# Performance work log

Measured on AMD Instinct MI355X. Metric: run time of the kernel, lower is better.

The kernel has to match this reference:

```python
import jax, jax.numpy as jnp
import numpy as np
from jax import lax


def setup_inputs() -> dict:
    key = jax.random.key(0)
    ks = jax.random.split(key, 16)
    def rn(k, shape, s=0.05):
        return (jax.random.normal(k, shape) * s).astype(jnp.float32)
    B, N, F = 16, 1024, 200
    return dict(
        x=jax.random.normal(ks[0], (B, 1, N, F), dtype=jnp.float32),
        gat_W=rn(ks[1], (F, F)), att_src=rn(ks[2], (F,)), att_dst=rn(ks[3], (F,)), gat_b=rn(ks[4], (F,)),
        conv1_w=rn(ks[5], (40, 1, 1, 26)), conv1_b=rn(ks[6], (40,)),
        bn1_g=jnp.ones((40,), jnp.float32), bn1_b=jnp.zeros((40,), jnp.float32),
        bn1_m=jnp.zeros((40,), jnp.float32), bn1_v=jnp.ones((40,), jnp.float32),
        conv2_w=rn(ks[7], (40, 40, N), 0.01), conv2_b=rn(ks[8], (40,)),
        bn2_g=jnp.ones((40,), jnp.float32), bn2_b=jnp.zeros((40,), jnp.float32),
        bn2_m=jnp.zeros((40,), jnp.float32), bn2_v=jnp.ones((40,), jnp.float32),
        projc_w=rn(ks[9], (40, 40)), projc_b=rn(ks[10], (40,)),
        W1=rn(ks[11], (1400, 1024)), b1=rn(ks[12], (1024,)),
        W2=rn(ks[13], (1024, 1024)), b2=rn(ks[14], (1024,)),
        ln_g=jnp.ones((1024,), jnp.float32), ln_b=jnp.zeros((1024,), jnp.float32),
    )


def _bn(y, g, b, m, v, eps=1e-5):
    # eval-mode BatchNorm over channel axis 1
    shp = (1, -1) + (1,) * (y.ndim - 2)
    return (y - m.reshape(shp)) * (g.reshape(shp) / jnp.sqrt(v.reshape(shp) + eps)) + b.reshape(shp)


def reference(x, gat_W, att_src, att_dst, gat_b, conv1_w, conv1_b,
              bn1_g, bn1_b, bn1_m, bn1_v, conv2_w, conv2_b,
              bn2_g, bn2_b, bn2_m, bn2_v, projc_w, projc_b,
              W1, b1, W2, b2, ln_g, ln_b):
    B, _, N, F = x.shape  # (16,1,1024,200)
    # --- EEG_GAT (PyG GATConv, heads=1). edge_index only covers nodes 0..N-1;
    # add_self_loops applies to all B*N nodes -> first graph is dense attention
    # (complete graph incl. self), remaining nodes see only their self-loop.
    h = x.reshape(B * N, F) @ gat_W               # (B*N, 200)
    a_s = h[:N] @ att_src                          # source scores, first graph
    a_d = h[:N] @ att_dst                          # target scores
    logits = jax.nn.leaky_relu(a_s[None, :] + a_d[:, None], 0.2)  # [target i, source j]
    out0 = jax.nn.softmax(logits, axis=1) @ h[:N]  # (N, 200)
    gat = (jnp.concatenate([out0, h[N:]], axis=0) + gat_b).reshape(B, 1, N, F)
    x = x + gat  # ResidualAdd (dropout in eval = identity)
    # --- PatchEmbedding shallownet
    y = lax.conv_general_dilated(x, conv1_w, (1, 1), 'VALID',
                                 dimension_numbers=('NCHW', 'OIHW', 'NCHW'))
    y = y + conv1_b[None, :, None, None]           # (B,40,1024,175)
    y = y.reshape(B, 40, N, 35, 5).mean(-1)        # AvgPool2d (1,5) stride (1,5)
    y = jax.nn.elu(_bn(y, bn1_g, bn1_b, bn1_m, bn1_v))
    y = jnp.einsum('bchw,och->bow', y, conv2_w) + conv2_b[None, :, None]  # Conv2d(40,40,(1024,1)) -> (B,40,35)
    y = jax.nn.elu(_bn(y, bn2_g, bn2_b, bn2_m, bn2_v))
    # projection 1x1 conv then rearrange 'b e h w -> b (h w) e' then flatten
    y = jnp.einsum('bow,eo->bew', y, projc_w) + projc_b[None, :, None]
    y = y.transpose(0, 2, 1).reshape(B, -1)        # (B, 1400)
    # --- Proj_eeg
    z = y @ W1 + b1
    z = z + (jax.nn.gelu(z, approximate=False) @ W2 + b2)
    mu = z.mean(-1, keepdims=True)
    var = ((z - mu) ** 2).mean(-1, keepdims=True)
    return (z - mu) / jnp.sqrt(var + 1e-5) * ln_g + ln_b
```

## Files before the change

### kernel.cpp

```cpp
#include <hip/hip_runtime.h>
#include <math.h>

typedef __attribute__((ext_vector_type(8))) short short8;
typedef __attribute__((ext_vector_type(4))) float f32x4;

__device__ __forceinline__ unsigned f2bf(float f) {
  unsigned u = __float_as_uint(f);
  return (u + 0x7FFFu + ((u >> 16) & 1u)) >> 16;
}
__device__ __forceinline__ unsigned pk2(float lo, float hi) {
  return f2bf(lo) | (f2bf(hi) << 16);
}

#define WS_X1    0
#define WS_W2P   3328000
#define WS_AS    4966400
#define WS_AD    4967424
#define WS_WEFB  4968464
#define WS_S1    4969664
#define WS_SH1   4969704
#define WS_S2    4969744
#define WS_SH2   4969784
#define WS_H     4970496
#define WS_P     5232640
#define WS_HT    5494784
#define WS_AP    6281216
#define WS_Y3P   WS_P
#define WS_Y4    8378368
#define WS_Y5    8400768
#define WS_ZP    8455936
#define WS_Z2P   8570624
#define WS_WPT   8701696

__global__ __launch_bounds__(256) void k0_prep(const float* __restrict__ gat_W,
                        const float* __restrict__ conv1_w, const float* __restrict__ conv1_b,
                        const float* __restrict__ bn1_g, const float* __restrict__ bn1_b,
                        const float* __restrict__ bn1_m, const float* __restrict__ bn1_v,
                        const float* __restrict__ conv2_b,
                        const float* __restrict__ bn2_g, const float* __restrict__ bn2_b,
                        const float* __restrict__ bn2_m, const float* __restrict__ bn2_v,
                        const float* __restrict__ w2,
                        float* __restrict__ ws) {
  int bx = blockIdx.x, t = threadIdx.x;
  if (bx < 224) {
    unsigned short* wpt = (unsigned short*)(ws + WS_WPT);
    int idx = bx * 256 + t;
    int n = idx / 224, k = idx % 224;
    float v = (n < 200 && k < 200) ? gat_W[k * 200 + n] : 0.f;
    wpt[idx] = (unsigned short)f2bf(v);
    return;
  }
  if (bx == 224) {
    if (t < 48) {
      unsigned short* wb = (unsigned short*)(ws + WS_WEFB);
      float wv[30];
      if (t < 40) {
        for (int j = 0; j < 30; ++j) {
          float s = 0.f;
          for (int tt = 0; tt < 5; ++tt) {
            int k = j - tt;
            if (k >= 0 && k < 26) s += conv1_w[t * 26 + k];
          }
          wv[j] = s * 0.2f;
        }
      }
      for (int k = 0; k < 32; ++k)
        wb[t * 32 + k] = (unsigned short)f2bf((t < 40 && k < 30) ? wv[k] : 0.f);
    }
    if (t < 40) {
      float s1 = bn1_g[t] * rsqrtf(bn1_v[t] + 1e-5f);
      ws[WS_S1 + t] = s1;
      ws[WS_SH1 + t] = bn1_b[t] + (conv1_b[t] - bn1_m[t]) * s1;
      float s2 = bn2_g[t] * rsqrtf(bn2_v[t] + 1e-5f);
      ws[WS_S2 + t] = s2;
      ws[WS_SH2 + t] = bn2_b[t] + (conv2_b[t] - bn2_m[t]) * s2;
    }
    return;
  }
  __shared__ unsigned short lds[2560];
  int q = bx - 225;
  int c8 = q / 6, o0 = (q % 6) * 8;
  unsigned short* w2p = (unsigned short*)(ws + WS_W2P);
#pragma unroll
  for (int i = 0; i < 10; ++i) {
    int e = i * 256 + t;
    int o = e / 320, rr = e % 320;
    int c = rr / 8, nl = rr % 8;
    int oa = o0 + o;
    float v = (oa < 40) ? w2[(oa * 40 + c) * 1024 + c8 * 8 + nl] : 0.f;
    lds[o * 320 + nl * 40 + c] = (unsigned short)f2bf(v);
  }
  __syncthreads();
  uint4* src = (uint4*)lds;
  uint4* dst = (uint4*)(w2p + (c8 * 48 + o0) * 320);
  for (int i = t; i < 320; i += 256) dst[i] = src[i];
}

__global__ __launch_bounds__(256) void k1_mfma(const float* __restrict__ x,
                                               const unsigned short* __restrict__ wpt,
                                               const float* __restrict__ gat_b,
                                               float* __restrict__ h,
                                               unsigned short* __restrict__ hT,
                                               float* __restrict__ x1) {
  __shared__ unsigned short As[64 * 232];
  __shared__ unsigned short Bt[64 * 232];
  int t = threadIdx.x;
  int wave = t >> 6, lane = t & 63;
  int m16 = lane & 15, quad = lane >> 4;
  int row0 = blockIdx.x * 64;
  {
    int m = t >> 2, kq = (t & 3) * 8;
    const float* xr = x + (row0 + m) * 200;
#pragma unroll
    for (int s = 0; s < 7; ++s) {
      int kg = s * 32 + kq;
      uint4 pv;
      if (kg + 8 <= 200) {
        float4 a = *(const float4*)(xr + kg);
        float4 b = *(const float4*)(xr + kg + 4);
        pv.x = pk2(a.x, a.y); pv.y = pk2(a.z, a.w);
        pv.z = pk2(b.x, b.y); pv.w = pk2(b.z, b.w);
      } else {
        float e[8];
#pragma unroll
        for (int q = 0; q < 8; ++q) e[q] = (kg + q < 200) ? xr[kg + q] : 0.f;
        pv.x = pk2(e[0], e[1]); pv.y = pk2(e[2], e[3]);
        pv.z = pk2(e[4], e[5]); pv.w = pk2(e[6], e[7]);
      }
      *(uint4*)&As[m * 232 + kg] = pv;
    }
  }
  __syncthreads();
  for (int c = 0; c < 4; ++c) {
    int n0 = c * 64;
    for (int i = t; i < 1792; i += 256) {
      int row = i / 28, ch = i % 28;
      *(short8*)&Bt[row * 232 + ch * 8] = *(const short8*)&wpt[(n0 + row) * 224 + ch * 8];
    }
    __syncthreads();
    f32x4 acc[4];
#pragma unroll
    for (int nt = 0; nt < 4; ++nt) acc[nt] = (f32x4){0.f, 0.f, 0.f, 0.f};
#pragma unroll
    for (int s = 0; s < 7; ++s) {
      short8 af = *(const short8*)&As[(wave * 16 + m16) * 232 + s * 32 + quad * 8];
      int kb = s * 32 + quad * 8;
#pragma unroll
      for (int nt = 0; nt < 4; ++nt) {
        short8 bf = *(const short8*)&Bt[(nt * 16 + m16) * 232 + kb];
        acc[nt] = __builtin_amdgcn_mfma_f32_16x16x32_bf16(af, bf, acc[nt], 0, 0, 0);
      }
    }
    if (blockIdx.x < 16) {
#pragma unroll
      for (int nt = 0; nt < 4; ++nt) {
        int col = n0 + nt * 16 + m16;
#pragma unroll
        for (int r = 0; r < 4; ++r) {
          int row = row0 + wave * 16 + quad * 4 + r;
          float v = acc[nt][r];
          h[row * 256 + col] = v;
          hT[col * 1024 + row] = (unsigned short)f2bf(v);
        }
      }
    } else {
#pragma unroll
      for (int nt = 0; nt < 4; ++nt) {
        int col = n0 + nt * 16 + m16;
        if (col < 200) {
          float gb = gat_b[col];
#pragma unroll
          for (int r = 0; r < 4; ++r) {
            int row = row0 + wave * 16 + quad * 4 + r;
            x1[row * 200 + col] = x[row * 200 + col] + acc[nt][r] + gb;
          }
        }
      }
    }
    __syncthreads();
  }
}

__global__ __launch_bounds__(256) void k1b_scores(const float* __restrict__ h,
                                                  const float* __restrict__ att_src,
                                                  const float* __restrict__ att_dst,
                                                  float* __restrict__ as_,
                                                  float* __restrict__ ad_) {
  int t = threadIdx.x;
  int wave = t >> 6, lane = t & 63;
  int r = blockIdx.x * 4 + wave;
  float s = 0.f, d = 0.f;
  if (lane < 50) {
    float4 v = *(const float4*)(h + r * 256 + lane * 4);
    float4 a = *(const float4*)(att_src + lane * 4);
    float4 dd = *(const float4*)(att_dst + lane * 4);
    s = v.x * a.x + v.y * a.y + v.z * a.z + v.w * a.w;
    d = v.x * dd.x + v.y * dd.y + v.z * dd.z + v.w * dd.w;
  }
#pragma unroll
  for (int off = 32; off > 0; off >>= 1) {
    s += __shfl_down(s, off);
    d += __shfl_down(d, off);
  }
  if (lane == 0) {
    as_[r] = s;
    ad_[r] = d;
  }
}

__global__ __launch_bounds__(256) void kP(const float* __restrict__ as_,
                                          const float* __restrict__ ad_,
                                          unsigned short* __restrict__ Pb) {
  __shared__ float rb[256];
  int t = threadIdx.x, i = blockIdx.x;
  float a0 = as_[t], a1 = as_[256 + t], a2 = as_[512 + t], a3 = as_[768 + t];
  rb[t] = fmaxf(fmaxf(a0, a1), fmaxf(a2, a3));
  __syncthreads();
  for (int st = 128; st > 0; st >>= 1) {
    if (t < st) rb[t] = fmaxf(rb[t], rb[t + st]);
    __syncthreads();
  }
  float maxs = rb[0];
  __syncthreads();
  float ad = ad_[i];
  float mv = maxs + ad;
  float M = mv >= 0.f ? mv : 0.2f * mv;
  float av[4] = {a0, a1, a2, a3};
  float p[4];
  float s = 0.f;
#pragma unroll
  for (int q = 0; q < 4; ++q) {
    float v = av[q] + ad;
    float l = v >= 0.f ? v : 0.2f * v;
    p[q] = __expf(l - M);
    s += p[q];
  }
  rb[t] = s;
  __syncthreads();
  for (int st = 128; st > 0; st >>= 1) {
    if (t < st) rb[t] += rb[t + st];
    __syncthreads();
  }
  float inv = 1.f / rb[0];
#pragma unroll
  for (int q = 0; q < 4; ++q)
    Pb[i * 1024 + q * 256 + t] = (unsigned short)f2bf(p[q] * inv);
}

__global__ __launch_bounds__(256) void kAttn(const unsigned short* __restrict__ Pb,
                                             const unsigned short* __restrict__ hT,
                                             float* __restrict__ ap) {
  int t = threadIdx.x;
  int wave = t >> 6, lane = t & 63;
  int l15 = lane & 15, quad = lane >> 4;
  int i0 = blockIdx.x * 64, f0 = blockIdx.y * 64, j0 = blockIdx.z * 128;
  int arow = i0 + wave * 16 + l15;
  f32x4 acc[4];
#pragma unroll
  for (int nt = 0; nt < 4; ++nt) acc[nt] = (f32x4){0.f, 0.f, 0.f, 0.f};
#pragma unroll
  for (int ks = 0; ks < 4; ++ks) {
    int koff = j0 + ks * 32 + quad * 8;
    short8 a = *(const short8*)&Pb[arow * 1024 + koff];
#pragma unroll
    for (int nt = 0; nt < 4; ++nt) {
      short8 bf = *(const short8*)&hT[(f0 + nt * 16 + l15) * 1024 + koff];
      acc[nt] = __builtin_amdgcn_mfma_f32_16x16x32_bf16(a, bf, acc[nt], 0, 0, 0);
    }
  }
#pragma unroll
  for (int nt = 0; nt < 4; ++nt)
#pragma unroll
    for (int r = 0; r < 4; ++r) {
      int row = i0 + wave * 16 + quad * 4 + r;
      ap[(blockIdx.z * 1024 + row) * 256 + f0 + nt * 16 + l15] = acc[nt][r];
    }
}

__global__ __launch_bounds__(256) void kAttnRed(const float* __restrict__ ap,
                                                const float* __restrict__ x,
                                                const float* __restrict__ gat_b,
                                                float* __restrict__ x1) {
  int t = threadIdx.x, r = blockIdx.x;
  if (t >= 200) return;
  float s = 0.f;
#pragma unroll
  for (int z = 0; z < 8; ++z) s += ap[(z * 1024 + r) * 256 + t];
  x1[r * 200 + t] = x[r * 200 + t] + s + gat_b[t];
}

__global__ __launch_bounds__(320, 2) void k3_conv(const float* __restrict__ x1,
                                                  const unsigned short* __restrict__ w2pre,
                                                  const unsigned short* __restrict__ weffB,
                                                  const float* __restrict__ ws,
                                                  float* __restrict__ y3p) {
  __shared__ __align__(16) char smem[48448];
  float* xbp = (float*)smem;
  unsigned short* tA = (unsigned short*)(smem + 6400);
  unsigned short* t2 = (unsigned short*)(smem + 24832);
  int t = threadIdx.x;
  int b = blockIdx.x, nc = blockIdx.y;
  int n0 = nc * 8;
  int wave = t >> 6, lane = t & 63;
  int l15 = lane & 15, quad = lane >> 4;
  for (int i = t; i < 400; i += 320) {
    int nn = i / 50, q = i % 50;
    ((float4*)(xbp + nn * 200))[q] = ((const float4*)(x1 + (b * 1024 + n0 + nn) * 200))[q];
  }
  __syncthreads();
  if (t < 280) {
    int nn = t / 35, p = t % 35;
    const float* xr = xbp + nn * 200 + p * 5;
    uint pv[16];
#pragma unroll
    for (int kk = 0; kk < 15; ++kk) pv[kk] = pk2(xr[kk * 2], xr[kk * 2 + 1]);
    pv[15] = 0u;
    uint4* dst = (uint4*)(tA + t * 32);
    dst[0] = make_uint4(pv[0], pv[1], pv[2], pv[3]);
    dst[1] = make_uint4(pv[4], pv[5], pv[6], pv[7]);
    dst[2] = make_uint4(pv[8], pv[9], pv[10], pv[11]);
    dst[3] = make_uint4(pv[12], pv[13], pv[14], pv[15]);
  } else if (t < 288) {
    uint4 z = make_uint4(0u, 0u, 0u, 0u);
    uint4* dst = (uint4*)(tA + t * 32);
    dst[0] = z; dst[1] = z; dst[2] = z; dst[3] = z;
  }
  __syncthreads();
  {
    int mt0 = wave * 4;
    int nmt = wave < 4 ? 4 : 2;
    short8 bw[3];
    float s1v[3] = {0.f, 0.f, 0.f}, sh1v[3] = {0.f, 0.f, 0.f};
#pragma unroll
    for (int nt = 0; nt < 3; ++nt) {
      bw[nt] = *(const short8*)&weffB[(nt * 16 + l15) * 32 + quad * 8];
      int c = nt * 16 + l15;
      if (c < 40) {
        s1v[nt] = ws[WS_S1 + c];
        sh1v[nt] = ws[WS_SH1 + c];
      }
    }
    for (int mi = 0; mi < nmt; ++mi) {
      int mt = mt0 + mi;
      short8 a = *(const short8*)&tA[(mt * 16 + l15) * 32 + quad * 8];
#pragma unroll
      for (int nt = 0; nt < 3; ++nt) {
        int c = nt * 16 + l15;
        if (c >= 40) continue;
        f32x4 c4 = {0.f, 0.f, 0.f, 0.f};
        c4 = __builtin_amdgcn_mfma_f32_16x16x32_bf16(a, bw[nt], c4, 0, 0, 0);
#pragma unroll
        for (int r = 0; r < 4; ++r) {
          int m = mt * 16 + quad * 4 + r;
          if (m < 280) {
            float v = c4[r] * s1v[nt] + sh1v[nt];
            float e = v > 0.f ? v : __expf(v) - 1.f;
            int p = m % 35, nn = m / 35;
            t2[p * 328 + nn * 40 + c] = (unsigned short)f2bf(e);
          }
        }
      }
    }
  }
  __syncthreads();
  f32x4 acc[3][3];
#pragma unroll
  for (int mt = 0; mt < 3; ++mt)
#pragma unroll
    for (int nt = 0; nt < 3; ++nt) acc[mt][nt] = (f32x4){0.f, 0.f, 0.f, 0.f};
  const unsigned short* bbase = w2pre + nc * 48 * 320;
#pragma unroll
  for (int ks = 0; ks < 2; ++ks) {
    int koff = wave * 64 + ks * 32 + quad * 8;
    short8 a[3], bb[3];
#pragma unroll
    for (int mt = 0; mt < 3; ++mt) {
      int row = mt * 16 + l15;
      row = row > 35 ? 35 : row;
      a[mt] = *(const short8*)&t2[row * 328 + koff];
    }
#pragma unroll
    for (int nt = 0; nt < 3; ++nt)
      bb[nt] = *(const short8*)&bbase[(nt * 16 + l15) * 320 + koff];
#pragma unroll
    for (int mt = 0; mt < 3; ++mt)
#pragma unroll
      for (int nt = 0; nt < 3; ++nt)
        acc[mt][nt] = __builtin_amdgcn_mfma_f32_16x16x32_bf16(a[mt], bb[nt], acc[mt][nt], 0, 0, 0);
  }
  __syncthreads();
  float* red0 = (float*)smem;
  float* red1 = red0 + 48 * 49;
  if (wave < 2) {
    float* r = wave ? red1 : red0;
#pragma unroll
    for (int mt = 0; mt < 3; ++mt)
#pragma unroll
      for (int nt = 0; nt < 3; ++nt)
#pragma unroll
        for (int q = 0; q < 4; ++q)
          r[(mt * 16 + quad * 4 + q) * 49 + nt * 16 + l15] = acc[mt][nt][q];
  }
  __syncthreads();
  if (wave == 2 || wave == 3) {
    float* r = (wave == 3) ? red1 : red0;
#pragma unroll
    for (int mt = 0; mt < 3; ++mt)
#pragma unroll
      for (int nt = 0; nt < 3; ++nt)
#pragma unroll
        for (int q = 0; q < 4; ++q)
          r[(mt * 16 + quad * 4 + q) * 49 + nt * 16 + l15] += acc[mt][nt][q];
  }
  __syncthreads();
  if (wave == 4) {
#pragma unroll
    for (int mt = 0; mt < 3; ++mt)
#pragma unroll
      for (int nt = 0; nt < 3; ++nt)
#pragma unroll
        for (int q = 0; q < 4; ++q)
          red0[(mt * 16 + quad * 4 + q) * 49 + nt * 16 + l15] += acc[mt][nt][q];
  }
  __syncthreads();
  float* dst = y3p + (b * 128 + nc) * 1400;
  for (int idx = t; idx < 1400; idx += 320) {
    int o = idx / 35, p = idx % 35;
    dst[idx] = red0[p * 49 + o] + red1[p * 49 + o];
  }
}

__global__ __launch_bounds__(256) void k4a_red(const float* __restrict__ y3p,
                                               const float* __restrict__ ws,
                                               float* __restrict__ y4) {
  int t = threadIdx.x;
  if (t >= 200) return;
  int b = blockIdx.x;
  int idx = blockIdx.y * 200 + t;
  float s = 0.f;
#pragma unroll 4
  for (int q = 0; q < 128; ++q) s += y3p[(b * 128 + q) * 1400 + idx];
  int o = idx / 35;
  float v = s * ws[WS_S2 + o] + ws[WS_SH2 + o];
  y4[b * 1400 + idx] = v > 0.f ? v : __expf(v) - 1.f;
}

__global__ __launch_bounds__(256) void k4b_proj(const float* __restrict__ y4,
                                                const float* __restrict__ projc_w,
                                                const float* __restrict__ projc_b,
                                                float* __restrict__ y5) {
  __shared__ __align__(16) float tls[1400];
  int t = threadIdx.x, b = blockIdx.x;
  for (int i = t; i < 350; i += 256)
    ((float4*)tls)[i] = ((const float4*)(y4 + b * 1400))[i];
  __syncthreads();
  for (int idx = t; idx < 1400; idx += 256) {
    int p = idx / 40, e = idx % 40;
    float acc = projc_b[e];
    for (int o = 0; o < 40; ++o) acc += tls[o * 35 + p] * projc_w[e * 40 + o];
    y5[b * 1400 + idx] = acc;
  }
}

__global__ __launch_bounds__(256) void k5_fc1(const float* __restrict__ y5,
                                              const float* __restrict__ W1,
                                              float* __restrict__ zp) {
  __shared__ __align__(16) float yls[3200];
  int t = threadIdx.x;
  int nc = blockIdx.x, kc = blockIdx.y;
  for (int i = t; i < 800; i += 256) {
    int bb = i / 50, q = i % 50;
    ((float4*)yls)[bb * 50 + q] = *(const float4*)(y5 + bb * 1400 + kc * 200 + q * 4);
  }
  __syncthreads();
  int nl = t & 31, bg = t >> 5;
  int n = nc * 32 + nl;
  float acc0 = 0.f, acc1 = 0.f;
  const float* y0 = yls + (bg * 2) * 200;
  const float* y1 = yls + (bg * 2 + 1) * 200;
  for (int k = 0; k < 200; ++k) {
    float w = W1[(kc * 200 + k) * 1024 + n];
    acc0 += y0[k] * w;
    acc1 += y1[k] * w;
  }
  zp[(kc * 16 + bg * 2) * 1024 + n] = acc0;
  zp[(kc * 16 + bg * 2 + 1) * 1024 + n] = acc1;
}

__global__ __launch_bounds__(256) void k6_fc2(const float* __restrict__ zp,
                                              const float* __restrict__ b1,
                                              const float* __restrict__ W2,
                                              float* __restrict__ z2p) {
  __shared__ __align__(16) float gls[2048];
  int t = threadIdx.x;
  int nc = blockIdx.x, kc = blockIdx.y;
  for (int i = t; i < 2048; i += 256) {
    int bb = i >> 7, kk = i & 127;
    int np = kc * 128 + kk;
    float s = b1[np];
#pragma unroll
    for (int j = 0; j < 7; ++j) s += zp[(j * 16 + bb) * 1024 + np];
    gls[i] = 0.5f * s * (1.f + erff(s * 0.70710678f));
  }
  __syncthreads();
  int nl = t & 31, bg = t >> 5;
  int n = nc * 32 + nl;
  float acc0 = 0.f, acc1 = 0.f;
  const float* g0 = gls + (bg * 2) * 128;
  const float* g1 = gls + (bg * 2 + 1) * 128;
  for (int k = 0; k < 128; ++k) {
    float w = W2[(kc * 128 + k) * 1024 + n];
    acc0 += g0[k] * w;
    acc1 += g1[k] * w;
  }
  z2p[(kc * 16 + bg * 2) * 1024 + n] = acc0;
  z2p[(kc * 16 + bg * 2 + 1) * 1024 + n] = acc1;
}

__global__ __launch_bounds__(256) void k7_ln(const float* __restrict__ zp,
                                             const float* __restrict__ z2p,
                                             const float* __restrict__ b1,
                                             const float* __restrict__ b2,
                                             const float* __restrict__ ln_g,
                                             const float* __restrict__ ln_b,
                                             float* __restrict__ out) {
  __shared__ float r1[256], r2[256];
  int t = threadIdx.x, b = blockIdx.x;
  float4 v = *(const float4*)(b1 + t * 4);
  float4 bb2 = *(const float4*)(b2 + t * 4);
  v.x += bb2.x; v.y += bb2.y; v.z += bb2.z; v.w += bb2.w;
#pragma unroll
  for (int kc = 0; kc < 7; ++kc) {
    float4 p = *(const float4*)(zp + (kc * 16 + b) * 1024 + t * 4);
    v.x += p.x; v.y += p.y; v.z += p.z; v.w += p.w;
  }
#pragma unroll
  for (int kc = 0; kc < 8; ++kc) {
    float4 p = *(const float4*)(z2p + (kc * 16 + b) * 1024 + t * 4);
    v.x += p.x; v.y += p.y; v.z += p.z; v.w += p.w;
  }
  r1[t] = v.x + v.y + v.z + v.w;
  r2[t] = v.x * v.x + v.y * v.y + v.z * v.z + v.w * v.w;
  __syncthreads();
  for (int s = 128; s > 0; s >>= 1) {
    if (t < s) {
      r1[t] += r1[t + s];
      r2[t] += r2[t + s];
    }
    __syncthreads();
  }
  float mu = r1[0] * (1.f / 1024.f);
  float var = r2[0] * (1.f / 1024.f) - mu * mu;
  float rstd = rsqrtf(var + 1e-5f);
  float4 gg = *(const float4*)(ln_g + t * 4);
  float4 bb = *(const float4*)(ln_b + t * 4);
  float4 o;
  o.x = (v.x - mu) * rstd * gg.x + bb.x;
  o.y = (v.y - mu) * rstd * gg.y + bb.y;
  o.z = (v.z - mu) * rstd * gg.z + bb.z;
  o.w = (v.w - mu) * rstd * gg.w + bb.w;
  *(float4*)(out + b * 1024 + t * 4) = o;
}

extern "C" void kernel_launch(void* const* d_in, const int* in_sizes, int n_in,
                              void* d_out, int out_size, void* d_ws, size_t ws_size,
                              hipStream_t stream) {
  (void)in_sizes; (void)n_in; (void)out_size; (void)ws_size;
  const float* x       = (const float*)d_in[0];
  const float* gat_W   = (const float*)d_in[1];
  const float* att_src = (const float*)d_in[2];
  const float* att_dst = (const float*)d_in[3];
  const float* gat_b   = (const float*)d_in[4];
  const float* conv1_w = (const float*)d_in[5];
  const float* conv2_w = (const float*)d_in[11];
  const float* projc_w = (const float*)d_in[17];
  const float* projc_b = (const float*)d_in[18];
  const float* W1      = (const float*)d_in[19];
  const float* b1      = (const float*)d_in[20];
  const float* W2      = (const float*)d_in[21];
  const float* b2      = (const float*)d_in[22];
  const float* ln_g    = (const float*)d_in[23];
  const float* ln_b    = (const float*)d_in[24];
  float* ws  = (float*)d_ws;
  float* out = (float*)d_out;

  hipLaunchKernelGGL(k0_prep, dim3(993), dim3(256), 0, stream, gat_W, conv1_w,
                     (const float*)d_in[6], (const float*)d_in[7], (const float*)d_in[8],
                     (const float*)d_in[9], (const float*)d_in[10], (const float*)d_in[12],
                     (const float*)d_in[13], (const float*)d_in[14], (const float*)d_in[15],
                     (const float*)d_in[16], conv2_w, ws);
  hipLaunchKernelGGL(k1_mfma, dim3(256), dim3(256), 0, stream, x,
                     (const unsigned short*)(ws + WS_WPT), gat_b, ws + WS_H,
                     (unsigned short*)(ws + WS_HT), ws + WS_X1);
  hipLaunchKernelGGL(k1b_scores, dim3(256), dim3(256), 0, stream, ws + WS_H, att_src, att_dst,
                     ws + WS_AS, ws + WS_AD);
  hipLaunchKernelGGL(kP, dim3(1024), dim3(256), 0, stream, ws + WS_AS, ws + WS_AD,
                     (unsigned short*)(ws + WS_P));
  hipLaunchKernelGGL(kAttn, dim3(16, 4, 8), dim3(256), 0, stream,
                     (const unsigned short*)(ws + WS_P),
                     (const unsigned short*)(ws + WS_HT), ws + WS_AP);
  hipLaunchKernelGGL(kAttnRed, dim3(1024), dim3(256), 0, stream, ws + WS_AP, x, gat_b,
                     ws + WS_X1);
  hipLaunchKernelGGL(k3_conv, dim3(16, 128), dim3(320), 0, stream, ws + WS_X1,
                     (const unsigned short*)(ws + WS_W2P),
                     (const unsigned short*)(ws + WS_WEFB), ws, ws + WS_Y3P);
  hipLaunchKernelGGL(k4a_red, dim3(16, 7), dim3(256), 0, stream, ws + WS_Y3P, ws, ws + WS_Y4);
  hipLaunchKernelGGL(k4b_proj, dim3(16), dim3(256), 0, stream, ws + WS_Y4, projc_w, projc_b,
                     ws + WS_Y5);
  hipLaunchKernelGGL(k5_fc1, dim3(32, 7), dim3(256), 0, stream, ws + WS_Y5, W1, ws + WS_ZP);
  hipLaunchKernelGGL(k6_fc2, dim3(32, 8), dim3(256), 0, stream, ws + WS_ZP, b1, W2,
                     ws + WS_Z2P);
  hipLaunchKernelGGL(k7_ln, dim3(16), dim3(256), 0, stream, ws + WS_ZP, ws + WS_Z2P, b1, b2,
                     ln_g, ln_b, out);
}
```

Measured before the change: 235.4 us.

## Remove split-K partials in attention and conv, fusing reductions into consumers

The attention GEMM now loops over the full K range in each block and writes x + attention + bias straight to x1, which drops the partial-sum buffer and the separate reduction kernel. The conv kernel handles four 8-row chunks per block, with shared memory reused between stages, so it writes a quarter as many partials. The reduction and BN/ELU step is merged into the projection kernel, removing another launch. The tradeoff is less parallelism: attention runs on only 64 blocks and conv on 512, and the fused k4 runs 16 blocks, each summing 32 partials serially.

```diff
diff --git a/kernel.cpp b/kernel.cpp
--- a/kernel.cpp
+++ b/kernel.cpp
@@ -24,9 +24,7 @@
 #define WS_H     4970496
 #define WS_P     5232640
 #define WS_HT    5494784
-#define WS_AP    6281216
 #define WS_Y3P   WS_P
-#define WS_Y4    8378368
 #define WS_Y5    8400768
 #define WS_ZP    8455936
 #define WS_Z2P   8570624
@@ -249,18 +247,20 @@
 
 __global__ __launch_bounds__(256) void kAttn(const unsigned short* __restrict__ Pb,
                                              const unsigned short* __restrict__ hT,
-                                             float* __restrict__ ap) {
+                                             const float* __restrict__ x,
+                                             const float* __restrict__ gat_b,
+                                             float* __restrict__ x1) {
   int t = threadIdx.x;
   int wave = t >> 6, lane = t & 63;
   int l15 = lane & 15, quad = lane >> 4;
-  int i0 = blockIdx.x * 64, f0 = blockIdx.y * 64, j0 = blockIdx.z * 128;
+  int i0 = blockIdx.x * 64, f0 = blockIdx.y * 64;
   int arow = i0 + wave * 16 + l15;
   f32x4 acc[4];
 #pragma unroll
   for (int nt = 0; nt < 4; ++nt) acc[nt] = (f32x4){0.f, 0.f, 0.f, 0.f};
-#pragma unroll
-  for (int ks = 0; ks < 4; ++ks) {
-    int koff = j0 + ks * 32 + quad * 8;
+#pragma unroll 4
+  for (int ks = 0; ks < 32; ++ks) {
+    int koff = ks * 32 + quad * 8;
     short8 a = *(const short8*)&Pb[arow * 1024 + koff];
 #pragma unroll
     for (int nt = 0; nt < 4; ++nt) {
@@ -269,24 +269,17 @@
     }
   }
 #pragma unroll
-  for (int nt = 0; nt < 4; ++nt)
-#pragma unroll
-    for (int r = 0; r < 4; ++r) {
-      int row = i0 + wave * 16 + quad * 4 + r;
-      ap[(blockIdx.z * 1024 + row) * 256 + f0 + nt * 16 + l15] = acc[nt][r];
-    }
-}
-
-__global__ __launch_bounds__(256) void kAttnRed(const float* __restrict__ ap,
-                                                const float* __restrict__ x,
-                                                const float* __restrict__ gat_b,
-                                                float* __restrict__ x1) {
-  int t = threadIdx.x, r = blockIdx.x;
-  if (t >= 200) return;
-  float s = 0.f;
-#pragma unroll
-  for (int z = 0; z < 8; ++z) s += ap[(z * 1024 + r) * 256 + t];
-  x1[r * 200 + t] = x[r * 200 + t] + s + gat_b[t];
+  for (int nt = 0; nt < 4; ++nt) {
+    int col = f0 + nt * 16 + l15;
+    if (col < 200) {
+      float gb = gat_b[col];
+#pragma unroll
+      for (int r = 0; r < 4; ++r) {
+        int row = i0 + wave * 16 + quad * 4 + r;
+        x1[row * 200 + col] = x[row * 200 + col] + acc[nt][r] + gb;
+      }
+    }
+  }
 }
 
 __global__ __launch_bounds__(320, 2) void k3_conv(const float* __restrict__ x1,
@@ -294,66 +287,79 @@
                                                   const unsigned short* __restrict__ weffB,
                                                   const float* __restrict__ ws,
                                                   float* __restrict__ y3p) {
-  __shared__ __align__(16) char smem[48448];
+  __shared__ __align__(16) char smem[30016];
   float* xbp = (float*)smem;
   unsigned short* tA = (unsigned short*)(smem + 6400);
-  unsigned short* t2 = (unsigned short*)(smem + 24832);
+  unsigned short* t2 = (unsigned short*)(smem + 6400);
   int t = threadIdx.x;
   int b = blockIdx.x, nc = blockIdx.y;
-  int n0 = nc * 8;
   int wave = t >> 6, lane = t & 63;
   int l15 = lane & 15, quad = lane >> 4;
-  for (int i = t; i < 400; i += 320) {
-    int nn = i / 50, q = i % 50;
-    ((float4*)(xbp + nn * 200))[q] = ((const float4*)(x1 + (b * 1024 + n0 + nn) * 200))[q];
-  }
-  __syncthreads();
-  if (t < 280) {
-    int nn = t / 35, p = t % 35;
-    const float* xr = xbp + nn * 200 + p * 5;
-    uint pv[16];
-#pragma unroll
-    for (int kk = 0; kk < 15; ++kk) pv[kk] = pk2(xr[kk * 2], xr[kk * 2 + 1]);
-    pv[15] = 0u;
-    uint4* dst = (uint4*)(tA + t * 32);
-    dst[0] = make_uint4(pv[0], pv[1], pv[2], pv[3]);
-    dst[1] = make_uint4(pv[4], pv[5], pv[6], pv[7]);
-    dst[2] = make_uint4(pv[8], pv[9], pv[10], pv[11]);
-    dst[3] = make_uint4(pv[12], pv[13], pv[14], pv[15]);
-  } else if (t < 288) {
-    uint4 z = make_uint4(0u, 0u, 0u, 0u);
-    uint4* dst = (uint4*)(tA + t * 32);
-    dst[0] = z; dst[1] = z; dst[2] = z; dst[3] = z;
-  }
-  __syncthreads();
+  short8 bw[3];
+  float s1v[3], sh1v[3];
+#pragma unroll
+  for (int nt = 0; nt < 3; ++nt) {
+    bw[nt] = *(const short8*)&weffB[(nt * 16 + l15) * 32 + quad * 8];
+    int c = nt * 16 + l15;
+    s1v[nt] = (c < 40) ? ws[WS_S1 + c] : 0.f;
+    sh1v[nt] = (c < 40) ? ws[WS_SH1 + c] : 0.f;
+  }
+  f32x4 acc[3][3];
+#pragma unroll
+  for (int mt = 0; mt < 3; ++mt)
+#pragma unroll
+    for (int nt = 0; nt < 3; ++nt) acc[mt][nt] = (f32x4){0.f, 0.f, 0.f, 0.f};
+  int mt0 = wave * 4;
+  int nmt = wave < 4 ? 4 : 2;
   {
-    int mt0 = wave * 4;
-    int nmt = wave < 4 ? 4 : 2;
-    short8 bw[3];
-    float s1v[3] = {0.f, 0.f, 0.f}, sh1v[3] = {0.f, 0.f, 0.f};
-#pragma unroll
-    for (int nt = 0; nt < 3; ++nt) {
-      bw[nt] = *(const short8*)&weffB[(nt * 16 + l15) * 32 + quad * 8];
-      int c = nt * 16 + l15;
-      if (c < 40) {
-        s1v[nt] = ws[WS_S1 + c];
-        sh1v[nt] = ws[WS_SH1 + c];
-      }
-    }
+    int n0 = nc * 32;
+    for (int i = t; i < 400; i += 320) {
+      int nn = i / 50, q = i % 50;
+      ((float4*)(xbp + nn * 200))[q] = ((const float4*)(x1 + (b * 1024 + n0 + nn) * 200))[q];
+    }
+  }
+  __syncthreads();
+  for (int it = 0; it < 4; ++it) {
+    int c8 = nc * 4 + it;
+    if (t < 280) {
+      int nn = t / 35, p = t % 35;
+      const float* xr = xbp + nn * 200 + p * 5;
+      uint pv[16];
+#pragma unroll
+      for (int kk = 0; kk < 15; ++kk) pv[kk] = pk2(xr[kk * 2], xr[kk * 2 + 1]);
+      pv[15] = 0u;
+      uint4* dst = (uint4*)(tA + t * 32);
+      dst[0] = make_uint4(pv[0], pv[1], pv[2], pv[3]);
+      dst[1] = make_uint4(pv[4], pv[5], pv[6], pv[7]);
+      dst[2] = make_uint4(pv[8], pv[9], pv[10], pv[11]);
+      dst[3] = make_uint4(pv[12], pv[13], pv[14], pv[15]);
+    } else if (t < 288) {
+      uint4 z = make_uint4(0u, 0u, 0u, 0u);
+      uint4* dst = (uint4*)(tA + t * 32);
+      dst[0] = z; dst[1] = z; dst[2] = z; dst[3] = z;
+    }
+    __syncthreads();
+    f32x4 c4[4][3];
+    for (int mi = 0; mi < nmt; ++mi) {
+      short8 a = *(const short8*)&tA[((mt0 + mi) * 16 + l15) * 32 + quad * 8];
+#pragma unroll
+      for (int nt = 0; nt < 3; ++nt) {
+        f32x4 z = {0.f, 0.f, 0.f, 0.f};
+        c4[mi][nt] = __builtin_amdgcn_mfma_f32_16x16x32_bf16(a, bw[nt], z, 0, 0, 0);
+      }
+    }
+    __syncthreads();
     for (int mi = 0; mi < nmt; ++mi) {
       int mt = mt0 + mi;
-      short8 a = *(const short8*)&tA[(mt * 16 + l15) * 32 + quad * 8];
 #pragma unroll
       for (int nt = 0; nt < 3; ++nt) {
         int c = nt * 16 + l15;
         if (c >= 40) continue;
-        f32x4 c4 = {0.f, 0.f, 0.f, 0.f};
-        c4 = __builtin_amdgcn_mfma_f32_16x16x32_bf16(a, bw[nt], c4, 0, 0, 0);
 #pragma unroll
         for (int r = 0; r < 4; ++r) {
           int m = mt * 16 + quad * 4 + r;
           if (m < 280) {
-            float v = c4[r] * s1v[nt] + sh1v[nt];
+            float v = c4[mi][nt][r] * s1v[nt] + sh1v[nt];
             float e = v > 0.f ? v : __expf(v) - 1.f;
             int p = m % 35, nn = m / 35;
             t2[p * 328 + nn * 40 + c] = (unsigned short)f2bf(e);
@@ -361,34 +367,36 @@
         }
       }
     }
-  }
-  __syncthreads();
-  f32x4 acc[3][3];
-#pragma unroll
-  for (int mt = 0; mt < 3; ++mt)
-#pragma unroll
-    for (int nt = 0; nt < 3; ++nt) acc[mt][nt] = (f32x4){0.f, 0.f, 0.f, 0.f};
-  const unsigned short* bbase = w2pre + nc * 48 * 320;
-#pragma unroll
-  for (int ks = 0; ks < 2; ++ks) {
-    int koff = wave * 64 + ks * 32 + quad * 8;
-    short8 a[3], bb[3];
-#pragma unroll
-    for (int mt = 0; mt < 3; ++mt) {
-      int row = mt * 16 + l15;
-      row = row > 35 ? 35 : row;
-      a[mt] = *(const short8*)&t2[row * 328 + koff];
-    }
-#pragma unroll
-    for (int nt = 0; nt < 3; ++nt)
-      bb[nt] = *(const short8*)&bbase[(nt * 16 + l15) * 320 + koff];
-#pragma unroll
-    for (int mt = 0; mt < 3; ++mt)
+    __syncthreads();
+    if (it < 3) {
+      int n0n = nc * 32 + (it + 1) * 8;
+      for (int i = t; i < 400; i += 320) {
+        int nn = i / 50, q = i % 50;
+        ((float4*)(xbp + nn * 200))[q] = ((const float4*)(x1 + (b * 1024 + n0n + nn) * 200))[q];
+      }
+    }
+    const unsigned short* bbase = w2pre + c8 * 48 * 320;
+#pragma unroll
+    for (int ks = 0; ks < 2; ++ks) {
+      int koff = wave * 64 + ks * 32 + quad * 8;
+      short8 a[3], bb[3];
+#pragma unroll
+      for (int mt = 0; mt < 3; ++mt) {
+        int row = mt * 16 + l15;
+        row = row > 35 ? 35 : row;
+        a[mt] = *(const short8*)&t2[row * 328 + koff];
+      }
 #pragma unroll
       for (int nt = 0; nt < 3; ++nt)
-        acc[mt][nt] = __builtin_amdgcn_mfma_f32_16x16x32_bf16(a[mt], bb[nt], acc[mt][nt], 0, 0, 0);
-  }
-  __syncthreads();
+        bb[nt] = *(const short8*)&bbase[(nt * 16 + l15) * 320 + koff];
+#pragma unroll
+      for (int mt = 0; mt < 3; ++mt)
+#pragma unroll
+        for (int nt = 0; nt < 3; ++nt)
+          acc[mt][nt] = __builtin_amdgcn_mfma_f32_16x16x32_bf16(a[mt], bb[nt], acc[mt][nt], 0, 0, 0);
+    }
+    __syncthreads();
+  }
   float* red0 = (float*)smem;
   float* red1 = red0 + 48 * 49;
   if (wave < 2) {
@@ -423,36 +431,28 @@
           red0[(mt * 16 + quad * 4 + q) * 49 + nt * 16 + l15] += acc[mt][nt][q];
   }
   __syncthreads();
-  float* dst = y3p + (b * 128 + nc) * 1400;
+  float* dst = y3p + (b * 32 + nc) * 1400;
   for (int idx = t; idx < 1400; idx += 320) {
     int o = idx / 35, p = idx % 35;
     dst[idx] = red0[p * 49 + o] + red1[p * 49 + o];
   }
 }
 
-__global__ __launch_bounds__(256) void k4a_red(const float* __restrict__ y3p,
-                                               const float* __restrict__ ws,
-                                               float* __restrict__ y4) {
-  int t = threadIdx.x;
-  if (t >= 200) return;
-  int b = blockIdx.x;
-  int idx = blockIdx.y * 200 + t;
-  float s = 0.f;
-#pragma unroll 4
-  for (int q = 0; q < 128; ++q) s += y3p[(b * 128 + q) * 1400 + idx];
-  int o = idx / 35;
-  float v = s * ws[WS_S2 + o] + ws[WS_SH2 + o];
-  y4[b * 1400 + idx] = v > 0.f ? v : __expf(v) - 1.f;
-}
-
-__global__ __launch_bounds__(256) void k4b_proj(const float* __restrict__ y4,
+__global__ __launch_bounds__(256) void k4_fused(const float* __restrict__ y3p,
+                                                const float* __restrict__ ws,
                                                 const float* __restrict__ projc_w,
                                                 const float* __restrict__ projc_b,
                                                 float* __restrict__ y5) {
-  __shared__ __align__(16) float tls[1400];
+  __shared__ float tls[1400];
   int t = threadIdx.x, b = blockIdx.x;
-  for (int i = t; i < 350; i += 256)
-    ((float4*)tls)[i] = ((const float4*)(y4 + b * 1400))[i];
+  for (int idx = t; idx < 1400; idx += 256) {
+    float s = 0.f;
+#pragma unroll 4
+    for (int q = 0; q < 32; ++q) s += y3p[(b * 32 + q) * 1400 + idx];
+    int o = idx / 35;
+    float v = s * ws[WS_S2 + o] + ws[WS_SH2 + o];
+    tls[idx] = v > 0.f ? v : __expf(v) - 1.f;
+  }
   __syncthreads();
   for (int idx = t; idx < 1400; idx += 256) {
     int p = idx / 40, e = idx % 40;
@@ -596,17 +596,14 @@
                      ws + WS_AS, ws + WS_AD);
   hipLaunchKernelGGL(kP, dim3(1024), dim3(256), 0, stream, ws + WS_AS, ws + WS_AD,
                      (unsigned short*)(ws + WS_P));
-  hipLaunchKernelGGL(kAttn, dim3(16, 4, 8), dim3(256), 0, stream,
+  hipLaunchKernelGGL(kAttn, dim3(16, 4), dim3(256), 0, stream,
                      (const unsigned short*)(ws + WS_P),
-                     (const unsigned short*)(ws + WS_HT), ws + WS_AP);
-  hipLaunchKernelGGL(kAttnRed, dim3(1024), dim3(256), 0, stream, ws + WS_AP, x, gat_b,
-                     ws + WS_X1);
-  hipLaunchKernelGGL(k3_conv, dim3(16, 128), dim3(320), 0, stream, ws + WS_X1,
+                     (const unsigned short*)(ws + WS_HT), x, gat_b, ws + WS_X1);
+  hipLaunchKernelGGL(k3_conv, dim3(16, 32), dim3(320), 0, stream, ws + WS_X1,
                      (const unsigned short*)(ws + WS_W2P),
                      (const unsigned short*)(ws + WS_WEFB), ws, ws + WS_Y3P);
-  hipLaunchKernelGGL(k4a_red, dim3(16, 7), dim3(256), 0, stream, ws + WS_Y3P, ws, ws + WS_Y4);
-  hipLaunchKernelGGL(k4b_proj, dim3(16), dim3(256), 0, stream, ws + WS_Y4, projc_w, projc_b,
-                     ws + WS_Y5);
+  hipLaunchKernelGGL(k4_fused, dim3(16), dim3(256), 0, stream, ws + WS_Y3P, ws, projc_w,
+                     projc_b, ws + WS_Y5);
   hipLaunchKernelGGL(k5_fc1, dim3(32, 7), dim3(256), 0, stream, ws + WS_Y5, W1, ws + WS_ZP);
   hipLaunchKernelGGL(k6_fc2, dim3(32, 8), dim3(256), 0, stream, ws + WS_ZP, b1, W2,
                      ws + WS_Z2P);
```

Result: slower. 310.7 us (+32.0%).
